# Kernel tuning notes

Measured on AMD Instinct MI355X. Metric: run time of the kernel, lower is better.

## Reference

```python
import jax, jax.numpy as jnp
import numpy as np

B, S, H, A, I = 64, 512, 1024, 1024, 1024


def setup_inputs() -> dict:
    key = jax.random.key(0)
    ks = jax.random.split(key, 12)
    s = lambda fan_in: 1.0 / np.sqrt(fan_in)
    return {
        "encoded": jax.random.normal(ks[0], (B, S, H), jnp.float32),
        "inputs": jax.random.normal(ks[1], (B, I), jnp.float32),
        "states": jax.random.normal(ks[2], (B, H), jnp.float32),
        # attention params
        "W_enc": jax.random.uniform(ks[3], (H, A), jnp.float32, -s(H), s(H)),
        "b_enc": jnp.zeros((A,), jnp.float32),
        "W_dec": jax.random.uniform(ks[4], (H, A), jnp.float32, -s(H), s(H)),
        "b_dec": jnp.zeros((A,), jnp.float32),
        "w_out": jax.random.uniform(ks[5], (A, 1), jnp.float32, -s(A), s(A)),
        "b_out": jnp.zeros((1,), jnp.float32),
        # GRU cell params (input size = I + H)
        "W_ih": jax.random.uniform(ks[6], (3 * H, I + H), jnp.float32, -s(H), s(H)),
        "W_hh": jax.random.uniform(ks[7], (3 * H, H), jnp.float32, -s(H), s(H)),
        "b_ih": jax.random.uniform(ks[8], (3 * H,), jnp.float32, -s(H), s(H)),
        "b_hh": jax.random.uniform(ks[9], (3 * H,), jnp.float32, -s(H), s(H)),
    }


def reference(encoded, inputs, states, W_enc, b_enc, W_dec, b_dec, w_out, b_out,
              W_ih, W_hh, b_ih, b_hh):
    # setup_memory: project encoder states  [B,S,H] @ [H,A] -> [B,S,A]
    enc_proj = jnp.einsum("bsh,ha->bsa", encoded, W_enc) + b_enc
    # project decoder state and broadcast over S
    dec_proj = states @ W_dec + b_dec                      # [B,A]
    projected = enc_proj + dec_proj[:, None, :]            # [B,S,A]
    scores = jnp.tanh(projected) @ w_out + b_out           # [B,S,1]
    weights = jax.nn.softmax(scores, axis=1)               # [B,S,1]
    attention = jnp.sum(encoded * weights, axis=1)         # [B,H]
    # GRU cell on concatenated input
    x = jnp.concatenate([inputs, attention], axis=1)       # [B,I+H]
    gi = x @ W_ih.T + b_ih                                 # [B,3H]
    gh = states @ W_hh.T + b_hh                            # [B,3H]
    i_r, i_z, i_n = jnp.split(gi, 3, axis=1)
    h_r, h_z, h_n = jnp.split(gh, 3, axis=1)
    r = jax.nn.sigmoid(i_r + h_r)
    z = jax.nn.sigmoid(i_z + h_z)
    n = jnp.tanh(i_n + r * h_n)
    return (1.0 - z) * n + z * states                      # [B,H]
```

## Files before the change

### kernel.cpp

```cpp
#include <hip/hip_runtime.h>
#include <stdint.h>

typedef __bf16 bf16x8 __attribute__((ext_vector_type(8)));
typedef float f32x4 __attribute__((ext_vector_type(4)));

#define LOG2E 1.4426950408889634f
#define LSTR 32

__device__ __forceinline__ unsigned short f2bf(float f) {
  unsigned int x = __builtin_bit_cast(unsigned int, f);
  x += 0x7FFFu + ((x >> 16) & 1u);
  return (unsigned short)(x >> 16);
}
__device__ __forceinline__ float tanh_fast(float x) {
  float cx = fminf(fmaxf(x, -15.f), 15.f);
  float e = __builtin_amdgcn_exp2f(cx * (2.f * LOG2E));
  return (e - 1.f) * __builtin_amdgcn_rcpf(e + 1.f);
}
__device__ __forceinline__ float sigmoid_fast(float x) {
  float cx = fminf(fmaxf(x, -30.f), 30.f);
  float e = __builtin_amdgcn_exp2f(cx * LOG2E);
  return e * __builtin_amdgcn_rcpf(e + 1.f);
}
__device__ __forceinline__ ushort4 cvt4(const float4 f) {
  return make_ushort4(f2bf(f.x), f2bf(f.y), f2bf(f.z), f2bf(f.w));
}
__device__ __forceinline__ bf16x8 cvt8(const f32x4 lo, const f32x4 hi) {
  union { unsigned short u[8]; bf16x8 v; } r;
  r.u[0] = f2bf(lo[0]); r.u[1] = f2bf(lo[1]);
  r.u[2] = f2bf(lo[2]); r.u[3] = f2bf(lo[3]);
  r.u[4] = f2bf(hi[0]); r.u[5] = f2bf(hi[1]);
  r.u[6] = f2bf(hi[2]); r.u[7] = f2bf(hi[3]);
  return r.v;
}

__device__ __forceinline__ void gl_lds16(const void* g, const void* lds_base) {
  __builtin_amdgcn_global_load_lds(
      (const __attribute__((address_space(1))) unsigned int*)(uintptr_t)g,
      (__attribute__((address_space(3))) unsigned int*)(unsigned int)(uintptr_t)lds_base,
      16, 0, 0);
}

__global__ __launch_bounds__(256) void k_prep(
    const float* __restrict__ W_enc, unsigned short* __restrict__ Wt,
    const float* __restrict__ states, const float* __restrict__ W_dec,
    const float* __restrict__ b_dec, const float* __restrict__ b_enc,
    float* __restrict__ dvec, float4* __restrict__ zbase) {
  __shared__ unsigned short tile[64][65];
  __shared__ float red[256];
  const int bid = blockIdx.x;
  const int tid = threadIdx.x;
  if (bid < 256) {
    const int bx = bid & 15, by = bid >> 4;
    const int x = tid & 63, y0 = tid >> 6;
#pragma unroll
    for (int i = y0; i < 64; i += 4)
      tile[i][x] = f2bf(W_enc[(size_t)(by * 64 + i) * 1024 + bx * 64 + x]);
    __syncthreads();
#pragma unroll
    for (int i = y0; i < 64; i += 4)
      Wt[(size_t)(bx * 64 + i) * 1024 + by * 64 + x] = tile[x][i];
  } else if (bid < 768) {
    const int bb = bid - 256;
    const int b = bb >> 3;
    const int a0 = (bb & 7) * 128;
    const int a = tid & 127, half = tid >> 7;
    const float* sp = states + (size_t)b * 1024;
    const float* wp = W_dec + a0 + a;
    float acc = 0.f;
    const int kb = half * 512;
#pragma unroll 8
    for (int k = kb; k < kb + 512; ++k)
      acc += sp[k] * wp[(size_t)k * 1024];
    red[tid] = acc;
    __syncthreads();
    if (tid < 128) {
      float v = red[tid] + red[tid + 128];
      dvec[(size_t)b * 1024 + a0 + tid] = v + b_dec[a0 + tid] + b_enc[a0 + tid];
    }
  } else {
    const float4 z = {0.f, 0.f, 0.f, 0.f};
    zbase[(size_t)(bid - 768) * 256 + tid] = z;
  }
}

__global__ __launch_bounds__(256, 3) void k_scoresF(
    const float* __restrict__ enc,
    const unsigned short* __restrict__ Wt,
    const float* __restrict__ dvec,
    const float* __restrict__ w_out,
    float* __restrict__ scores) {
  __shared__ alignas(16) unsigned char lds[2][24576];
  __shared__ float sc[128];

  const int tid = threadIdx.x;
  const int wave = tid >> 6, lane = tid & 63;
  const int l15 = lane & 15, quad = lane >> 4;
  const int xcd = blockIdx.x & 7;
  const int kb_ = blockIdx.x >> 3;
  const int mt = ((kb_ >> 3) << 3) | xcd;
  const int nt = kb_ & 7;
  const int row0 = mt * 128;
  const int b = row0 >> 9;
  const int wm = (wave >> 1) * 64, wn = (wave & 1) * 64;

  const int arow_lo = lane >> 3;
  const int csw = (lane & 7) ^ arow_lo;
  const float* srcA[4];
#pragma unroll
  for (int s = 0; s < 4; ++s) {
    const int g = wave * 4 + s;
    srcA[s] = enc + (size_t)(row0 + g * 8 + arow_lo) * 1024 + csw * 4;
  }
  const int srow = lane >> 2;
  const int fsw = ((lane >> 2) & 3) ^ ((lane >> 4) & 3);
  const int skoff = (((lane & 3) ^ fsw) * 8);
  const unsigned short* srcB[2];
#pragma unroll
  for (int s = 0; s < 2; ++s) {
    const int reg = wave * 2 + s;
    srcB[s] = Wt + (size_t)(nt * 128 + reg * 16 + srow) * 1024 + skoff;
  }
  const int rchunk = ((quad ^ ((l15 & 3) ^ ((l15 >> 2) & 3))) * 8);
  const int aslot0 = ((quad << 1) ^ (l15 & 7)) << 4;
  const int aslot1 = aslot0 ^ 16;

  if (tid < 128) sc[tid] = 0.f;

  const f32x4 vz = {0.f, 0.f, 0.f, 0.f};
  f32x4 acc[4][4];
#pragma unroll
  for (int i = 0; i < 4; ++i)
#pragma unroll
    for (int j = 0; j < 4; ++j) acc[i][j] = vz;

  auto STAGE = [&](int bi, int kk) {
    unsigned char* Ab = &lds[bi][0];
    unsigned char* Bb = &lds[bi][16384];
#pragma unroll
    for (int s = 0; s < 4; ++s)
      gl_lds16(srcA[s] + kk, Ab + (wave * 4 + s) * 1024);
#pragma unroll
    for (int s = 0; s < 2; ++s)
      gl_lds16(srcB[s] + kk, Bb + (wave * 2 + s) * 1024);
  };
  auto COMPUTE = [&](int bi) {
    const unsigned char* Ab = &lds[bi][0];
    const unsigned short* Bb = (const unsigned short*)&lds[bi][16384];
    bf16x8 af[4], bg[4];
#pragma unroll
    for (int i = 0; i < 4; ++i) {
      const unsigned char* ap = Ab + ((wm + i * 16 + l15) << 7);
      const f32x4 lo = *(const f32x4*)(ap + aslot0);
      const f32x4 hi = *(const f32x4*)(ap + aslot1);
      af[i] = cvt8(lo, hi);
    }
#pragma unroll
    for (int j = 0; j < 4; ++j)
      bg[j] = *(const bf16x8*)(Bb + (wn + j * 16 + l15) * LSTR + rchunk);
#pragma unroll
    for (int i = 0; i < 4; ++i)
#pragma unroll
      for (int j = 0; j < 4; ++j)
        acc[i][j] = __builtin_amdgcn_mfma_f32_16x16x32_bf16(af[i], bg[j],
                                                            acc[i][j], 0, 0, 0);
  };

  STAGE(0, 0);
  __syncthreads();

#pragma unroll 1
  for (int k0 = 0; k0 < 1024; k0 += 64) {
    STAGE(1, k0 + 32);
    COMPUTE(0);
    __syncthreads();
    if (k0 + 64 < 1024) { STAGE(0, k0 + 64); }
    COMPUTE(1);
    __syncthreads();
  }

  float p[4][4];
#pragma unroll
  for (int i = 0; i < 4; ++i)
#pragma unroll
    for (int r = 0; r < 4; ++r) p[i][r] = 0.f;
#pragma unroll
  for (int j = 0; j < 4; ++j) {
    const int a = nt * 128 + wn + j * 16 + l15;
    const float dv = dvec[(size_t)b * 1024 + a];
    const float wo = w_out[a];
#pragma unroll
    for (int i = 0; i < 4; ++i)
#pragma unroll
      for (int r = 0; r < 4; ++r)
        p[i][r] += tanh_fast(acc[i][j][r] + dv) * wo;
  }
#pragma unroll
  for (int i = 0; i < 4; ++i)
#pragma unroll
    for (int r = 0; r < 4; ++r) {
      float v = p[i][r];
      v += __shfl_xor(v, 1);
      v += __shfl_xor(v, 2);
      v += __shfl_xor(v, 4);
      v += __shfl_xor(v, 8);
      if (l15 == 0) atomicAdd(&sc[wm + i * 16 + quad * 4 + r], v);
    }
  __syncthreads();
  if (tid < 128)
    atomicAdd(&scores[(size_t)b * 512 + (row0 & 511) + tid], sc[tid]);
}

__global__ __launch_bounds__(256) void k_attn(const float* __restrict__ enc,
                                              const float* __restrict__ scores,
                                              float* __restrict__ att) {
  const int b = blockIdx.x >> 3;
  const int hch = blockIdx.x & 7;
  const int tid = threadIdx.x;
  __shared__ float w[512];
  __shared__ float redm[4], reds[4];
  __shared__ float red[16][132];

  const float s0 = scores[(size_t)b * 512 + tid];
  const float s1 = scores[(size_t)b * 512 + 256 + tid];
  float m = fmaxf(s0, s1);
#pragma unroll
  for (int off = 32; off; off >>= 1) m = fmaxf(m, __shfl_xor(m, off));
  const int wv = tid >> 6;
  if ((tid & 63) == 0) redm[wv] = m;
  __syncthreads();
  m = fmaxf(fmaxf(redm[0], redm[1]), fmaxf(redm[2], redm[3]));
  const float e0 = __builtin_amdgcn_exp2f((s0 - m) * LOG2E);
  const float e1 = __builtin_amdgcn_exp2f((s1 - m) * LOG2E);
  float sum = e0 + e1;
#pragma unroll
  for (int off = 32; off; off >>= 1) sum += __shfl_xor(sum, off);
  if ((tid & 63) == 0) reds[wv] = sum;
  __syncthreads();
  sum = reds[0] + reds[1] + reds[2] + reds[3];
  const float inv = 1.f / sum;
  w[tid] = e0 * inv;
  w[tid + 256] = e1 * inv;
  __syncthreads();

  const int sgrp = tid >> 4;
  const int hsub = tid & 15;
  const int h0 = hch * 128 + hsub * 8;
  float a[8];
#pragma unroll
  for (int j = 0; j < 8; ++j) a[j] = 0.f;
#pragma unroll 8
  for (int si = 0; si < 32; ++si) {
    const int s = si * 16 + sgrp;
    const float ws_ = w[s];
    const float* ep = enc + (size_t)(b * 512 + s) * 1024 + h0;
    const float4 v0 = *(const float4*)ep;
    const float4 v1 = *(const float4*)(ep + 4);
    a[0] += ws_ * v0.x; a[1] += ws_ * v0.y;
    a[2] += ws_ * v0.z; a[3] += ws_ * v0.w;
    a[4] += ws_ * v1.x; a[5] += ws_ * v1.y;
    a[6] += ws_ * v1.z; a[7] += ws_ * v1.w;
  }
#pragma unroll
  for (int j = 0; j < 8; ++j) red[sgrp][hsub * 8 + j] = a[j];
  __syncthreads();
#pragma unroll
  for (int step = 8; step >= 1; step >>= 1) {
    if (sgrp < step) {
#pragma unroll
      for (int j = 0; j < 8; ++j)
        red[sgrp][hsub * 8 + j] += red[sgrp + step][hsub * 8 + j];
    }
    __syncthreads();
  }
  if (sgrp == 0) {
    float4 o0 = {red[0][hsub * 8 + 0], red[0][hsub * 8 + 1],
                 red[0][hsub * 8 + 2], red[0][hsub * 8 + 3]};
    float4 o1 = {red[0][hsub * 8 + 4], red[0][hsub * 8 + 5],
                 red[0][hsub * 8 + 6], red[0][hsub * 8 + 7]};
    *(float4*)(att + (size_t)b * 1024 + h0) = o0;
    *(float4*)(att + (size_t)b * 1024 + h0 + 4) = o1;
  }
}

__global__ __launch_bounds__(256) void k_gru_gemm(
    const float* __restrict__ xin,
    const float* __restrict__ att,
    const float* __restrict__ states,
    const float* __restrict__ W_ih,
    const float* __restrict__ W_hh,
    float* __restrict__ gbuf) {
  const int tid = threadIdx.x;
  const int wave = tid >> 6, lane = tid & 63;
  const int l15 = lane & 15, quad = lane >> 4;
  const int kk = blockIdx.x & 3;
  const int rest = blockIdx.x >> 2;
  const bool is_gh = rest >= 48;
  const int nt = is_gh ? rest - 48 : rest;
  const int n0 = nt * 64;
  const int KT = is_gh ? 1024 : 2048;
  const int Kh = KT >> 2;
  const int kbase = kk * Kh;
  const float* W = is_gh ? W_hh : W_ih;
  const int plane = is_gh ? 4 + kk : kk;
  float* outp = gbuf + (size_t)plane * 64 * 3072;

  __shared__ alignas(16) unsigned short lA[64 * LSTR];
  __shared__ alignas(16) unsigned short lB[64 * LSTR];

  const f32x4 vz = {0.f, 0.f, 0.f, 0.f};
  f32x4 acc[2][2];
  acc[0][0] = vz; acc[0][1] = vz; acc[1][0] = vz; acc[1][1] = vz;

  const int arow = tid >> 2;
  const int achunk = (tid & 3) * 8;
  const int fswG = ((tid >> 2) & 3) ^ ((tid >> 4) & 3);
  const int wchunk = (((tid & 3) ^ fswG) * 8);
  const int rchunkG = ((quad ^ ((l15 & 3) ^ ((l15 >> 2) & 3))) * 8);
  const int wm2 = (wave >> 1) * 32, wn2 = (wave & 1) * 32;

  float4 ra0, ra1, rb0, rb1;
  auto LOADK = [&](int kg0) {
    const int kg = kg0 + achunk;
    const float* ap = is_gh ? (states + (size_t)arow * 1024 + kg)
                    : (kg < 1024 ? (xin + (size_t)arow * 1024 + kg)
                                 : (att + (size_t)arow * 1024 + (kg - 1024)));
    ra0 = *(const float4*)ap;
    ra1 = *(const float4*)(ap + 4);
    const float* wp = W + (size_t)(n0 + arow) * KT + kg;
    rb0 = *(const float4*)wp;
    rb1 = *(const float4*)(wp + 4);
  };
  LOADK(kbase);

#pragma unroll 1
  for (int k0 = 0; k0 < Kh; k0 += 32) {
    __syncthreads();
    *(ushort4*)(lA + arow * LSTR + wchunk) = cvt4(ra0);
    *(ushort4*)(lA + arow * LSTR + wchunk + 4) = cvt4(ra1);
    *(ushort4*)(lB + arow * LSTR + wchunk) = cvt4(rb0);
    *(ushort4*)(lB + arow * LSTR + wchunk + 4) = cvt4(rb1);
    __syncthreads();
    if (k0 + 32 < Kh) LOADK(kbase + k0 + 32);
    bf16x8 af[2], bg[2];
#pragma unroll
    for (int i = 0; i < 2; ++i)
      af[i] = *(const bf16x8*)(lA + (wm2 + i * 16 + l15) * LSTR + rchunkG);
#pragma unroll
    for (int j = 0; j < 2; ++j)
      bg[j] = *(const bf16x8*)(lB + (wn2 + j * 16 + l15) * LSTR + rchunkG);
#pragma unroll
    for (int i = 0; i < 2; ++i)
#pragma unroll
      for (int j = 0; j < 2; ++j)
        acc[i][j] = __builtin_amdgcn_mfma_f32_16x16x32_bf16(af[i], bg[j],
                                                            acc[i][j], 0, 0, 0);
  }
#pragma unroll
  for (int i = 0; i < 2; ++i)
#pragma unroll
    for (int j = 0; j < 2; ++j)
#pragma unroll
      for (int r = 0; r < 4; ++r) {
        const int m = wm2 + i * 16 + quad * 4 + r;
        const int n = n0 + wn2 + j * 16 + l15;
        outp[(size_t)m * 3072 + n] = acc[i][j][r];
      }
}

__global__ void k_gate(const float* __restrict__ gbuf,
                       const float* __restrict__ states,
                       const float* __restrict__ b_ih,
                       const float* __restrict__ b_hh,
                       float* __restrict__ outp) {
  const int idx = blockIdx.x * 256 + threadIdx.x;
  const int b = idx >> 10, h = idx & 1023;
  float gir = 0.f, giz = 0.f, gin = 0.f, ghr = 0.f, ghz = 0.f, ghn = 0.f;
#pragma unroll
  for (int p = 0; p < 4; ++p) {
    const float* gi = gbuf + ((size_t)p * 64 + b) * 3072;
    gir += gi[h]; giz += gi[1024 + h]; gin += gi[2048 + h];
    const float* gh = gbuf + ((size_t)(4 + p) * 64 + b) * 3072;
    ghr += gh[h]; ghz += gh[1024 + h]; ghn += gh[2048 + h];
  }
  const float ir = gir + b_ih[h];
  const float iz = giz + b_ih[1024 + h];
  const float in_ = gin + b_ih[2048 + h];
  const float hr = ghr + b_hh[h];
  const float hz = ghz + b_hh[1024 + h];
  const float hn = ghn + b_hh[2048 + h];
  const float r = sigmoid_fast(ir + hr);
  const float z = sigmoid_fast(iz + hz);
  const float n = tanh_fast(in_ + r * hn);
  const float hp = states[idx];
  outp[idx] = (1.f - z) * n + z * hp;
}

extern "C" void kernel_launch(void* const* d_in, const int* in_sizes, int n_in,
                              void* d_out, int out_size, void* d_ws, size_t ws_size,
                              hipStream_t stream) {
  const float* enc    = (const float*)d_in[0];
  const float* xin    = (const float*)d_in[1];
  const float* states = (const float*)d_in[2];
  const float* W_enc  = (const float*)d_in[3];
  const float* b_enc  = (const float*)d_in[4];
  const float* W_dec  = (const float*)d_in[5];
  const float* b_dec  = (const float*)d_in[6];
  const float* w_out  = (const float*)d_in[7];
  const float* W_ih   = (const float*)d_in[9];
  const float* W_hh   = (const float*)d_in[10];
  const float* b_ih   = (const float*)d_in[11];
  const float* b_hh   = (const float*)d_in[12];
  float* out = (float*)d_out;

  char* base = (char*)d_ws;
  unsigned short* Wt = (unsigned short*)base;
  float* dvec    = (float*)(base + 2097152);
  float* scoresb = (float*)(base + 2097152 + 262144);
  float* att     = (float*)(base + 2097152 + 262144 + 131072);
  float* gbuf    = (float*)(base + 2097152 + 262144 + 131072 + 262144);

  k_prep<<<800, 256, 0, stream>>>(W_enc, Wt, states, W_dec, b_dec, b_enc,
                                  dvec, (float4*)scoresb);
  k_scoresF<<<2048, 256, 0, stream>>>(enc, Wt, dvec, w_out, scoresb);
  k_attn<<<512, 256, 0, stream>>>(enc, scoresb, att);
  k_gru_gemm<<<384, 256, 0, stream>>>(xin, att, states, W_ih, W_hh, gbuf);
  k_gate<<<256, 256, 0, stream>>>(gbuf, states, b_ih, b_hh, out);
}
```

Baseline: 421.2 us.

## Split attention over sequence halves and double GRU split-K planes

The attention-weighted sum kernel now splits the sequence dimension into two halves, so it launches twice as many blocks and writes two partial attention vectors that the GRU GEMM adds while loading its A operand. The GRU GEMM split-K factor goes from 4 to 8, doubling the grid and the number of partial planes that the gate kernel reduces. The fp32-to-bf16 conversion in the scores kernel uses native __bf16 casts instead of manual rounding. This raises parallelism on small grids, at the cost of extra partial-sum traffic and more workspace.

```diff
diff --git a/kernel.cpp b/kernel.cpp
--- a/kernel.cpp
+++ b/kernel.cpp
@@ -25,13 +25,13 @@
 __device__ __forceinline__ ushort4 cvt4(const float4 f) {
   return make_ushort4(f2bf(f.x), f2bf(f.y), f2bf(f.z), f2bf(f.w));
 }
-__device__ __forceinline__ bf16x8 cvt8(const f32x4 lo, const f32x4 hi) {
-  union { unsigned short u[8]; bf16x8 v; } r;
-  r.u[0] = f2bf(lo[0]); r.u[1] = f2bf(lo[1]);
-  r.u[2] = f2bf(lo[2]); r.u[3] = f2bf(lo[3]);
-  r.u[4] = f2bf(hi[0]); r.u[5] = f2bf(hi[1]);
-  r.u[6] = f2bf(hi[2]); r.u[7] = f2bf(hi[3]);
-  return r.v;
+__device__ __forceinline__ bf16x8 cvt8c(const f32x4 lo, const f32x4 hi) {
+  bf16x8 r;
+  r[0] = (__bf16)lo[0]; r[1] = (__bf16)lo[1];
+  r[2] = (__bf16)lo[2]; r[3] = (__bf16)lo[3];
+  r[4] = (__bf16)hi[0]; r[5] = (__bf16)hi[1];
+  r[6] = (__bf16)hi[2]; r[7] = (__bf16)hi[3];
+  return r;
 }
 
 __device__ __forceinline__ void gl_lds16(const void* g, const void* lds_base) {
@@ -153,7 +153,7 @@
       const unsigned char* ap = Ab + ((wm + i * 16 + l15) << 7);
       const f32x4 lo = *(const f32x4*)(ap + aslot0);
       const f32x4 hi = *(const f32x4*)(ap + aslot1);
-      af[i] = cvt8(lo, hi);
+      af[i] = cvt8c(lo, hi);
     }
 #pragma unroll
     for (int j = 0; j < 4; ++j)
@@ -213,9 +213,10 @@
 
 __global__ __launch_bounds__(256) void k_attn(const float* __restrict__ enc,
                                               const float* __restrict__ scores,
-                                              float* __restrict__ att) {
-  const int b = blockIdx.x >> 3;
-  const int hch = blockIdx.x & 7;
+                                              float* __restrict__ att2) {
+  const int b = blockIdx.x >> 4;
+  const int hch = (blockIdx.x >> 1) & 7;
+  const int sh = blockIdx.x & 1;
   const int tid = threadIdx.x;
   __shared__ float w[512];
   __shared__ float redm[4], reds[4];
@@ -250,8 +251,8 @@
 #pragma unroll
   for (int j = 0; j < 8; ++j) a[j] = 0.f;
 #pragma unroll 8
-  for (int si = 0; si < 32; ++si) {
-    const int s = si * 16 + sgrp;
+  for (int si = 0; si < 16; ++si) {
+    const int s = sh * 256 + si * 16 + sgrp;
     const float ws_ = w[s];
     const float* ep = enc + (size_t)(b * 512 + s) * 1024 + h0;
     const float4 v0 = *(const float4*)ep;
@@ -274,18 +275,19 @@
     __syncthreads();
   }
   if (sgrp == 0) {
+    float* op = att2 + ((size_t)sh * 64 + b) * 1024 + h0;
     float4 o0 = {red[0][hsub * 8 + 0], red[0][hsub * 8 + 1],
                  red[0][hsub * 8 + 2], red[0][hsub * 8 + 3]};
     float4 o1 = {red[0][hsub * 8 + 4], red[0][hsub * 8 + 5],
                  red[0][hsub * 8 + 6], red[0][hsub * 8 + 7]};
-    *(float4*)(att + (size_t)b * 1024 + h0) = o0;
-    *(float4*)(att + (size_t)b * 1024 + h0 + 4) = o1;
+    *(float4*)op = o0;
+    *(float4*)(op + 4) = o1;
   }
 }
 
 __global__ __launch_bounds__(256) void k_gru_gemm(
     const float* __restrict__ xin,
-    const float* __restrict__ att,
+    const float* __restrict__ att2,
     const float* __restrict__ states,
     const float* __restrict__ W_ih,
     const float* __restrict__ W_hh,
@@ -293,16 +295,16 @@
   const int tid = threadIdx.x;
   const int wave = tid >> 6, lane = tid & 63;
   const int l15 = lane & 15, quad = lane >> 4;
-  const int kk = blockIdx.x & 3;
-  const int rest = blockIdx.x >> 2;
+  const int kk = blockIdx.x & 7;
+  const int rest = blockIdx.x >> 3;
   const bool is_gh = rest >= 48;
   const int nt = is_gh ? rest - 48 : rest;
   const int n0 = nt * 64;
   const int KT = is_gh ? 1024 : 2048;
-  const int Kh = KT >> 2;
+  const int Kh = KT >> 3;
   const int kbase = kk * Kh;
   const float* W = is_gh ? W_hh : W_ih;
-  const int plane = is_gh ? 4 + kk : kk;
+  const int plane = is_gh ? 8 + kk : kk;
   float* outp = gbuf + (size_t)plane * 64 * 3072;
 
   __shared__ alignas(16) unsigned short lA[64 * LSTR];
@@ -322,11 +324,22 @@
   float4 ra0, ra1, rb0, rb1;
   auto LOADK = [&](int kg0) {
     const int kg = kg0 + achunk;
-    const float* ap = is_gh ? (states + (size_t)arow * 1024 + kg)
-                    : (kg < 1024 ? (xin + (size_t)arow * 1024 + kg)
-                                 : (att + (size_t)arow * 1024 + (kg - 1024)));
-    ra0 = *(const float4*)ap;
-    ra1 = *(const float4*)(ap + 4);
+    if (is_gh) {
+      const float* ap = states + (size_t)arow * 1024 + kg;
+      ra0 = *(const float4*)ap;
+      ra1 = *(const float4*)(ap + 4);
+    } else if (kg < 1024) {
+      const float* ap = xin + (size_t)arow * 1024 + kg;
+      ra0 = *(const float4*)ap;
+      ra1 = *(const float4*)(ap + 4);
+    } else {
+      const float* p0 = att2 + (size_t)arow * 1024 + (kg - 1024);
+      const float* p1 = p0 + (size_t)64 * 1024;
+      const float4 x0 = *(const float4*)p0, y0 = *(const float4*)p1;
+      const float4 x1 = *(const float4*)(p0 + 4), y1 = *(const float4*)(p1 + 4);
+      ra0 = make_float4(x0.x + y0.x, x0.y + y0.y, x0.z + y0.z, x0.w + y0.w);
+      ra1 = make_float4(x1.x + y1.x, x1.y + y1.y, x1.z + y1.z, x1.w + y1.w);
+    }
     const float* wp = W + (size_t)(n0 + arow) * KT + kg;
     rb0 = *(const float4*)wp;
     rb1 = *(const float4*)(wp + 4);
@@ -377,10 +390,10 @@
   const int b = idx >> 10, h = idx & 1023;
   float gir = 0.f, giz = 0.f, gin = 0.f, ghr = 0.f, ghz = 0.f, ghn = 0.f;
 #pragma unroll
-  for (int p = 0; p < 4; ++p) {
+  for (int p = 0; p < 8; ++p) {
     const float* gi = gbuf + ((size_t)p * 64 + b) * 3072;
     gir += gi[h]; giz += gi[1024 + h]; gin += gi[2048 + h];
-    const float* gh = gbuf + ((size_t)(4 + p) * 64 + b) * 3072;
+    const float* gh = gbuf + ((size_t)(8 + p) * 64 + b) * 3072;
     ghr += gh[h]; ghz += gh[1024 + h]; ghn += gh[2048 + h];
   }
   const float ir = gir + b_ih[h];
@@ -417,13 +430,13 @@
   unsigned short* Wt = (unsigned short*)base;
   float* dvec    = (float*)(base + 2097152);
   float* scoresb = (float*)(base + 2097152 + 262144);
-  float* att     = (float*)(base + 2097152 + 262144 + 131072);
-  float* gbuf    = (float*)(base + 2097152 + 262144 + 131072 + 262144);
+  float* att2    = (float*)(base + 2097152 + 262144 + 131072);
+  float* gbuf    = (float*)(base + 2097152 + 262144 + 131072 + 524288);
 
   k_prep<<<800, 256, 0, stream>>>(W_enc, Wt, states, W_dec, b_dec, b_enc,
                                   dvec, (float4*)scoresb);
   k_scoresF<<<2048, 256, 0, stream>>>(enc, Wt, dvec, w_out, scoresb);
-  k_attn<<<512, 256, 0, stream>>>(enc, scoresb, att);
-  k_gru_gemm<<<384, 256, 0, stream>>>(xin, att, states, W_ih, W_hh, gbuf);
+  k_attn<<<1024, 256, 0, stream>>>(enc, scoresb, att2);
+  k_gru_gemm<<<768, 256, 0, stream>>>(xin, att2, states, W_ih, W_hh, gbuf);
   k_gate<<<256, 256, 0, stream>>>(gbuf, states, b_ih, b_hh, out);
 }
```

Result: no change. 426.1 us (+1.2%).
